# Performance work log

Measured on AMD Instinct MI355X. Metric: run time of the kernel, lower is better.

Reference implementation:

```python
import jax, jax.numpy as jnp
import numpy as np

B, T, D = 1, 4096, 2048
NUM_HEADS, NUM_KV_HEADS, HEAD_DIM = 16, 8, 128
QUERY_PRE_ATTN_SCALAR = HEAD_DIM ** -0.5
SOFT_CAP = 50.0
WINDOW = 1024
ROPE_BASE = 10000.0
ROPE_SCALE = 1.0
K_MASK = -2.3819763e+38


def apply_rope(x, positions, head_dim, max_wavelength=ROPE_BASE, scale_factor=ROPE_SCALE):
    # x: [B, T, N, H], positions: [B, T]
    fraction = 2.0 * jnp.arange(head_dim // 2, dtype=jnp.float32) / head_dim
    timescale = max_wavelength ** fraction  # [H/2]
    sinusoid = positions[..., None].astype(jnp.float32) / timescale  # [B, T, H/2]
    sinusoid = (sinusoid / scale_factor)[..., None, :]  # [B, T, 1, H/2]
    sin, cos = jnp.sin(sinusoid), jnp.cos(sinusoid)
    first, second = jnp.split(x, 2, axis=-1)
    out = jnp.concatenate([first * cos - second * sin,
                           second * cos + first * sin], axis=-1)
    return out.astype(x.dtype)


def setup_inputs() -> dict:
    key = jax.random.key(0)
    ks = jax.random.split(key, 4)
    x = jax.random.normal(ks[0], (B, T, D), dtype=jnp.float32)
    segment_pos = jnp.broadcast_to(jnp.arange(T, dtype=jnp.int32), (B, T))
    # causal mask [B, T, S]
    attn_mask = jnp.broadcast_to(
        jnp.tril(jnp.ones((T, T), dtype=jnp.bool_)), (B, T, T))
    q_w = jax.random.normal(ks[1], (NUM_HEADS, D, HEAD_DIM), dtype=jnp.float32) * 0.02
    kv_w = jax.random.normal(ks[2], (2, NUM_KV_HEADS, D, HEAD_DIM), dtype=jnp.float32) * 0.02
    o_w = jax.random.normal(ks[3], (NUM_HEADS, HEAD_DIM, D), dtype=jnp.float32) * 0.02
    return {"x": x, "segment_pos": segment_pos, "attn_mask": attn_mask,
            "q_w": q_w, "kv_w": kv_w, "o_w": o_w}


def reference(x, segment_pos, attn_mask, q_w, kv_w, o_w):
    # Projections (GQA: separate q and kv einsums)
    q = jnp.einsum('BTD,NDH->BTNH', x, q_w)          # [B,T,N,H]
    k = jnp.einsum('BSD,KDH->BSKH', x, kv_w[0])      # [B,S,K,H]
    v = jnp.einsum('BSD,KDH->BSKH', x, kv_w[1])      # [B,S,K,H]

    q = apply_rope(q, segment_pos, HEAD_DIM)
    q = q * QUERY_PRE_ATTN_SCALAR
    k = apply_rope(k, segment_pos, HEAD_DIM)

    num_groups = NUM_HEADS // NUM_KV_HEADS
    qg = q.reshape(B, T, NUM_KV_HEADS, num_groups, HEAD_DIM)
    logits = jnp.einsum('BTKGH,BSKH->BTKGS', qg, k)
    logits = logits.reshape(B, T, NUM_HEADS, -1)     # [B,T,N,S]

    # soft cap
    logits = jnp.tanh(logits / SOFT_CAP) * SOFT_CAP

    # sliding-window mask combined with causal mask
    all_ones = jnp.ones_like(attn_mask)
    sliding = jnp.triu(all_ones, -WINDOW + 1) * jnp.tril(all_ones, WINDOW - 1)
    mask = sliding * attn_mask                       # [B,T,S] bool

    padded = jnp.where(mask[:, :, None, :], logits, K_MASK)
    probs = jax.nn.softmax(padded, axis=-1).astype(k.dtype)

    probs_g = probs.reshape(B, T, NUM_KV_HEADS, num_groups, -1)
    encoded = jnp.einsum('BTKGS,BSKH->BTKGH', probs_g, v)
    encoded = encoded.reshape(B, T, NUM_HEADS, HEAD_DIM)

    attn_output = jnp.einsum('BTNH,NHD->BTD', encoded, o_w)
    return attn_output
```

## Files before the change

### kernel.cpp

```cpp
#include <hip/hip_runtime.h>
#include <hip/hip_bf16.h>
#include <math.h>

typedef __attribute__((ext_vector_type(8))) short short8;
typedef __attribute__((ext_vector_type(8))) unsigned short ushort8;
typedef __attribute__((ext_vector_type(4))) float f32x4;
typedef __attribute__((ext_vector_type(2))) float f32x2;

#define T_SEQ 4096
#define D_MODEL 2048
#define N_HEADS 16
#define N_KV 8
#define HEAD_DIM 128
#define QSCALE 0.08838834764831845f

__device__ __forceinline__ float bf2f(unsigned short u) {
  union { unsigned int i; float f; } x; x.i = ((unsigned int)u) << 16; return x.f;
}
__device__ __forceinline__ unsigned short f2bf(float f) {
  union { float f; unsigned int i; } x; x.f = f;
  unsigned int i = x.i;
  unsigned int r = i + 0x7fffu + ((i >> 16) & 1u);
  return (unsigned short)(r >> 16);
}

__global__ __launch_bounds__(256) void prep_kernel(const float* __restrict__ x,
                                                   unsigned short* __restrict__ xb,
                                                   const int* __restrict__ segpos,
                                                   float2* __restrict__ tab) {
  int b = blockIdx.x;
  if (b < 4096) {
    int idx = b * 256 + threadIdx.x;
    const float4* p = reinterpret_cast<const float4*>(x) + (size_t)idx * 2;
    float4 a = p[0], c = p[1];
    ushort8 o;
    o[0] = f2bf(a.x); o[1] = f2bf(a.y); o[2] = f2bf(a.z); o[3] = f2bf(a.w);
    o[4] = f2bf(c.x); o[5] = f2bf(c.y); o[6] = f2bf(c.z); o[7] = f2bf(c.w);
    reinterpret_cast<ushort8*>(xb)[idx] = o;
  } else {
    int idx = (b - 4096) * 256 + threadIdx.x;
    int t = idx >> 6, i = idx & 63;
    float pos = (float)segpos[t];
    float ts = powf(10000.f, (float)(2 * i) / 128.f);
    float ang = pos / ts;
    tab[idx] = make_float2(sinf(ang), cosf(ang));
  }
}

__global__ __launch_bounds__(256) void wqkv_transpose_kernel(const float* __restrict__ q_w,
                                                             const float* __restrict__ kv_w,
                                                             unsigned short* __restrict__ Wt) {
  __shared__ float tile[32][33];
  int z = blockIdx.z;
  const float* src = (z < 16) ? q_w + (size_t)z * 2048 * 128
                              : kv_w + (size_t)(z - 16) * 2048 * 128;
  unsigned short* dst = Wt + (size_t)z * 128 * 2048;
  int c0 = blockIdx.x * 32, r0 = blockIdx.y * 32;
  int tx = threadIdx.x & 31, ty = threadIdx.x >> 5;
#pragma unroll
  for (int i = 0; i < 4; ++i)
    tile[ty + i * 8][tx] = src[(size_t)(r0 + ty + i * 8) * 128 + c0 + tx];
  __syncthreads();
#pragma unroll
  for (int i = 0; i < 4; ++i)
    dst[(size_t)(c0 + ty + i * 8) * 2048 + r0 + tx] = f2bf(tile[tx][ty + i * 8]);
}

#define G2L(gp, lp)                                                           \
  __builtin_amdgcn_global_load_lds(                                           \
      (const __attribute__((address_space(1))) void*)(gp),                    \
      (__attribute__((address_space(3))) void*)(lp), 16, 0, 0)
#define GBAR() asm volatile("s_barrier" ::: "memory")
#define VMW(n) asm volatile("s_waitcnt vmcnt(" #n ")" ::: "memory")
#define LG0()  asm volatile("s_waitcnt lgkmcnt(0)" ::: "memory")

template <int OUT_BF16>
__global__ __launch_bounds__(512, 2) void gemm256_kernel(const unsigned short* __restrict__ A,
                                                         const unsigned short* __restrict__ Bt,
                                                         void* __restrict__ Cout,
                                                         int M, int N, int K) {
  extern __shared__ unsigned short smem[];
  unsigned short* ldsA = smem;
  unsigned short* ldsB = smem + 32768;
  const int tid = threadIdx.x;
  const int lane = tid & 63, wave = tid >> 6;
  const int wm = wave >> 2, wn = wave & 3;
  const int lr = lane & 15, lg = lane >> 4;
  const int swz = (lr & 7) << 3;
  const int c0s = (lg * 8) ^ swz;
  const int c1s = (32 + lg * 8) ^ swz;

  int id = blockIdx.y * gridDim.x + blockIdx.x;
  int nb = gridDim.x * gridDim.y;
  int sw = (id & 7) * (nb >> 3) + (id >> 3);
  const long brow = (long)(sw / gridDim.x) * 256;
  const long bcol = (long)(sw % gridDim.x) * 256;

  const unsigned short* Ag = A + brow * K;
  const unsigned short* Bg = Bt + bcol * K;

  const int r0 = tid >> 3;
  const int cs = ((tid & 7) * 8) ^ ((r0 & 7) << 3);

#define ST_A(tt, b, a)                                                        \
  { G2L(Ag + (size_t)((a) * 128 + r0) * K + (size_t)(tt) * 64 + cs,           \
        ldsA + (b) * 16384 + (a) * 8192 + tid * 8);                           \
    G2L(Ag + (size_t)((a) * 128 + r0 + 64) * K + (size_t)(tt) * 64 + cs,      \
        ldsA + (b) * 16384 + (a) * 8192 + 4096 + tid * 8); }
#define ST_B(tt, b, h)                                                        \
  { G2L(Bg + (size_t)((h) * 128 + r0) * K + (size_t)(tt) * 64 + cs,           \
        ldsB + (b) * 16384 + (h) * 8192 + tid * 8);                           \
    G2L(Bg + (size_t)((h) * 128 + r0 + 64) * K + (size_t)(tt) * 64 + cs,      \
        ldsB + (b) * 16384 + (h) * 8192 + 4096 + tid * 8); }

  f32x4 acc[8][4] = {};
  short8 bf[4][2];
  short8 af[4];

#define RD_B(b)                                                               \
  { const unsigned short* pb = ldsB + (b) * 16384 + wn * 4096;                \
    _Pragma("unroll")                                                         \
    for (int n = 0; n < 4; ++n) {                                             \
      bf[n][0] = *(const short8*)(pb + (n * 16 + lr) * 64 + c0s);             \
      bf[n][1] = *(const short8*)(pb + (n * 16 + lr) * 64 + c1s);             \
    } }
#define RD_A(b, mb)                                                           \
  { const unsigned short* pa = ldsA + (b) * 16384 + wm * 8192;                \
    af[0] = *(const short8*)(pa + ((mb) * 16 + lr) * 64 + c0s);               \
    af[1] = *(const short8*)(pa + ((mb) * 16 + lr) * 64 + c1s);               \
    af[2] = *(const short8*)(pa + ((mb) * 16 + 16 + lr) * 64 + c0s);          \
    af[3] = *(const short8*)(pa + ((mb) * 16 + 16 + lr) * 64 + c1s); }
#define MFMA2(mb)                                                             \
  { __builtin_amdgcn_s_setprio(1);                                            \
    _Pragma("unroll")                                                         \
    for (int n = 0; n < 4; ++n) {                                             \
      acc[mb][n]     = __builtin_amdgcn_mfma_f32_16x16x32_bf16(af[0], bf[n][0], acc[mb][n], 0, 0, 0);     \
      acc[mb][n]     = __builtin_amdgcn_mfma_f32_16x16x32_bf16(af[1], bf[n][1], acc[mb][n], 0, 0, 0);     \
      acc[mb + 1][n] = __builtin_amdgcn_mfma_f32_16x16x32_bf16(af[2], bf[n][0], acc[mb + 1][n], 0, 0, 0); \
      acc[mb + 1][n] = __builtin_amdgcn_mfma_f32_16x16x32_bf16(af[3], bf[n][1], acc[mb + 1][n], 0, 0, 0); \
    }                                                                         \
    __builtin_amdgcn_s_setprio(0); }

  const int NT = K >> 6;
  ST_B(0, 0, 0); ST_B(0, 0, 1); ST_A(0, 0, 0); ST_A(0, 0, 1);
  ST_B(1, 1, 0); ST_B(1, 1, 1);
  VMW(4); GBAR();
  for (int j = 0; j < (NT >> 1); ++j) {
    const int c1 = 2 * j + 1, t2 = 2 * j + 2, t3 = 2 * j + 3;
    const bool s2 = t2 < NT, s3 = t3 < NT;
    RD_B(0); RD_A(0, 0); ST_A(c1, 1, 0);
    GBAR(); LG0(); MFMA2(0); GBAR();
    RD_A(0, 2); ST_A(c1, 1, 1);
    if (s2) ST_B(t2, 0, 0);
    GBAR(); MFMA2(2); GBAR();
    RD_A(0, 4);
    if (s2) ST_B(t2, 0, 1);
    GBAR(); MFMA2(4); GBAR();
    RD_A(0, 6);
    if (s2) { VMW(4); } else { VMW(0); }
    GBAR(); LG0(); MFMA2(6); GBAR();
    RD_B(1); RD_A(1, 0);
    if (s2) ST_A(t2, 0, 0);
    GBAR(); LG0(); MFMA2(0); GBAR();
    RD_A(1, 2);
    if (s2) ST_A(t2, 0, 1);
    if (s3) ST_B(t3, 1, 0);
    GBAR(); MFMA2(2); GBAR();
    RD_A(1, 4);
    if (s3) ST_B(t3, 1, 1);
    GBAR(); MFMA2(4); GBAR();
    RD_A(1, 6);
    if (s3) { VMW(4); } else { VMW(0); }
    GBAR(); LG0(); MFMA2(6); GBAR();
  }

#pragma unroll
  for (int m = 0; m < 8; ++m) {
#pragma unroll
    for (int i = 0; i < 4; ++i) {
      long row = brow + wm * 128 + m * 16 + lg * 4 + i;
#pragma unroll
      for (int n = 0; n < 4; ++n) {
        long col = bcol + wn * 64 + n * 16 + lr;
        if (OUT_BF16)
          ((unsigned short*)Cout)[row * N + col] = f2bf(acc[m][n][i]);
        else
          ((float*)Cout)[row * N + col] = acc[m][n][i];
      }
    }
  }
#undef ST_A
#undef ST_B
#undef RD_A
#undef RD_B
#undef MFMA2
}

__global__ __launch_bounds__(512, 1) void gemm_op3_kernel(const unsigned short* __restrict__ A,
                                                          const unsigned short* __restrict__ Bt,
                                                          float* __restrict__ Cout,
                                                          int M, int N, int K) {
  extern __shared__ unsigned short smem[];
  unsigned short* ldsA = smem;
  unsigned short* ldsB = smem + 3 * 8192;
  const int tid = threadIdx.x;
  const int lane = tid & 63, wave = tid >> 6;
  const int wm = wave >> 2, wn = wave & 3;
  const int lr = lane & 15, lg = lane >> 4;
  const int swz = (lr & 7) << 3;
  const int c0s = (lg * 8) ^ swz;
  const int c1s = (32 + lg * 8) ^ swz;

  int id = blockIdx.y * gridDim.x + blockIdx.x;
  int sw = (id & 7) * 32 + (id >> 3);
  int c = sw >> 5, l = sw & 31;
  const long brow = (long)((c >> 2) * 16 + (l & 15)) * 128;
  const long bcol = (long)((c & 3) * 2 + (l >> 4)) * 256;

  const unsigned short* Ag = A + brow * K;
  const unsigned short* Bg = Bt + bcol * K;

  const int r0 = tid >> 3;
  const int cs = ((tid & 7) * 8) ^ ((r0 & 7) << 3);

#define ST_A3(tt, b)                                                          \
  { G2L(Ag + (size_t)(r0) * K + (size_t)(tt) * 64 + cs,                       \
        ldsA + (b) * 8192 + tid * 8);                                         \
    G2L(Ag + (size_t)(r0 + 64) * K + (size_t)(tt) * 64 + cs,                  \
        ldsA + (b) * 8192 + 4096 + tid * 8); }
#define ST_B3(tt, b, h)                                                       \
  { G2L(Bg + (size_t)((h) * 128 + r0) * K + (size_t)(tt) * 64 + cs,           \
        ldsB + (b) * 16384 + (h) * 8192 + tid * 8);                           \
    G2L(Bg + (size_t)((h) * 128 + r0 + 64) * K + (size_t)(tt) * 64 + cs,      \
        ldsB + (b) * 16384 + (h) * 8192 + 4096 + tid * 8); }

  f32x4 acc[4][4] = {};
  short8 bf[4][2];
  short8 af0[4], af1[4];

#define RD_B3(b)                                                              \
  { const unsigned short* pb = ldsB + (b) * 16384 + wn * 4096;                \
    _Pragma("unroll")                                                         \
    for (int n = 0; n < 4; ++n) {                                             \
      bf[n][0] = *(const short8*)(pb + (n * 16 + lr) * 64 + c0s);             \
      bf[n][1] = *(const short8*)(pb + (n * 16 + lr) * 64 + c1s);             \
    } }
#define RD_A3(b, mb, dst)                                                     \
  { const unsigned short* pa = ldsA + (b) * 8192 + wm * 4096;                 \
    dst[0] = *(const short8*)(pa + ((mb) * 16 + lr) * 64 + c0s);              \
    dst[1] = *(const short8*)(pa + ((mb) * 16 + lr) * 64 + c1s);              \
    dst[2] = *(const short8*)(pa + ((mb) * 16 + 16 + lr) * 64 + c0s);         \
    dst[3] = *(const short8*)(pa + ((mb) * 16 + 16 + lr) * 64 + c1s); }
#define MFMA2X(mb, afx)                                                       \
  { _Pragma("unroll")                                                         \
    for (int n = 0; n < 4; ++n) {                                             \
      acc[mb][n]     = __builtin_amdgcn_mfma_f32_16x16x32_bf16(afx[0], bf[n][0], acc[mb][n], 0, 0, 0);     \
      acc[mb][n]     = __builtin_amdgcn_mfma_f32_16x16x32_bf16(afx[1], bf[n][1], acc[mb][n], 0, 0, 0);     \
      acc[mb + 1][n] = __builtin_amdgcn_mfma_f32_16x16x32_bf16(afx[2], bf[n][0], acc[mb + 1][n], 0, 0, 0); \
      acc[mb + 1][n] = __builtin_amdgcn_mfma_f32_16x16x32_bf16(afx[3], bf[n][1], acc[mb + 1][n], 0, 0, 0); \
    } }

  const int NT = K >> 6;
  ST_B3(0, 0, 0); ST_B3(0, 0, 1); ST_A3(0, 0);
  ST_B3(1, 1, 0); ST_B3(1, 1, 1); ST_A3(1, 1);
  VMW(6); GBAR();
  int b = 0;
  for (int t = 0; t < NT; ++t) {
    int bn = b + 2; if (bn >= 3) bn -= 3;
    const bool st = (t + 2) < NT;
    RD_B3(b); RD_A3(b, 0, af0); RD_A3(b, 2, af1);
    if (st) { ST_B3(t + 2, bn, 0); ST_B3(t + 2, bn, 1); ST_A3(t + 2, bn); VMW(6); }
    else    { VMW(0); }
    GBAR(); LG0();
    __builtin_amdgcn_s_setprio(1);
    MFMA2X(0, af0); MFMA2X(2, af1);
    __builtin_amdgcn_s_setprio(0);
    GBAR();
    b = b + 1; if (b >= 3) b = 0;
  }

#pragma unroll
  for (int m = 0; m < 4; ++m) {
#pragma unroll
    for (int i = 0; i < 4; ++i) {
      long row = brow + wm * 64 + m * 16 + lg * 4 + i;
#pragma unroll
      for (int n = 0; n < 4; ++n) {
        long col = bcol + wn * 64 + n * 16 + lr;
        Cout[row * N + col] = acc[m][n][i];
      }
    }
  }
#undef ST_A3
#undef ST_B3
#undef RD_A3
#undef RD_B3
#undef MFMA2X
}

__global__ __launch_bounds__(256) void rope_vt_ow_kernel(const unsigned short* __restrict__ raw,
                                                         const float2* __restrict__ tab,
                                                         unsigned short* __restrict__ Qb,
                                                         unsigned short* __restrict__ Kb,
                                                         unsigned short* __restrict__ Vt,
                                                         const float* __restrict__ o_w,
                                                         unsigned short* __restrict__ o_wt) {
  __shared__ unsigned short tileU[32][33];
  __shared__ float tileF[32][33];
  int b = blockIdx.x;
  if (b < 3072) {
    int gid = b * 256 + threadIdx.x;
    int j = gid & 7;
    int rem = gid >> 3;
    int hs = rem % 24;
    int t = rem / 24;
    int i0 = j * 8;
    float sv[8], cv[8];
    const float2* tp = tab + t * 64 + i0;
#pragma unroll
    for (int q = 0; q < 8; ++q) { float2 sc2 = tp[q]; sv[q] = sc2.x; cv[q] = sc2.y; }
    if (hs < 16) {
      const unsigned short* p = raw + (size_t)t * 4096 + hs * 128 + i0;
      ushort8 a = *(const ushort8*)p;
      ushort8 c = *(const ushort8*)(p + 64);
      ushort8 o1, o2;
#pragma unroll
      for (int q = 0; q < 8; ++q) {
        float fa = bf2f(a[q]), fb = bf2f(c[q]);
        o1[q] = f2bf((fa * cv[q] - fb * sv[q]) * QSCALE);
        o2[q] = f2bf((fb * cv[q] + fa * sv[q]) * QSCALE);
      }
      unsigned short* qp = Qb + ((size_t)hs * T_SEQ + t) * 128 + i0;
      *(ushort8*)qp = o1;
      *(ushort8*)(qp + 64) = o2;
    } else {
      int kn = hs - 16;
      const unsigned short* p = raw + (size_t)t * 4096 + 2048 + kn * 128 + i0;
      ushort8 a = *(const ushort8*)p;
      ushort8 c = *(const ushort8*)(p + 64);
      ushort8 o1, o2;
#pragma unroll
      for (int q = 0; q < 8; ++q) {
        float fa = bf2f(a[q]), fb = bf2f(c[q]);
        o1[q] = f2bf(fa * cv[q] - fb * sv[q]);
        o2[q] = f2bf(fb * cv[q] + fa * sv[q]);
      }
      unsigned short* kp = Kb + ((size_t)kn * T_SEQ + t) * 128 + i0;
      *(ushort8*)kp = o1;
      *(ushort8*)(kp + 64) = o2;
    }
  } else if (b < 7168) {
    int id = b - 3072;
    int bx = id & 3, by = (id >> 2) & 127, bz = id >> 9;
    const unsigned short* src = raw + 3072 + (size_t)bz * 128;
    unsigned short* dst = Vt + (size_t)bz * 128 * 4096;
    int c0 = bx * 32, r0 = by * 32;
    int tx = threadIdx.x & 31, ty = threadIdx.x >> 5;
#pragma unroll
    for (int i = 0; i < 4; ++i)
      tileU[ty + i * 8][tx] = src[(size_t)(r0 + ty + i * 8) * 4096 + c0 + tx];
    __syncthreads();
#pragma unroll
    for (int i = 0; i < 4; ++i)
      dst[(size_t)(c0 + ty + i * 8) * 4096 + r0 + tx] = tileU[tx][ty + i * 8];
  } else {
    int id = b - 7168;
    int bx = id & 63, by = id >> 6;
    int c0 = bx * 32, r0 = by * 32;
    int tx = threadIdx.x & 31, ty = threadIdx.x >> 5;
#pragma unroll
    for (int i = 0; i < 4; ++i)
      tileF[ty + i * 8][tx] = o_w[(size_t)(r0 + ty + i * 8) * 2048 + c0 + tx];
    __syncthreads();
#pragma unroll
    for (int i = 0; i < 4; ++i)
      o_wt[(size_t)(c0 + ty + i * 8) * 2048 + r0 + tx] = f2bf(tileF[tx][ty + i * 8]);
  }
}

__global__ __launch_bounds__(512, 2) void attn_kernel(const unsigned short* __restrict__ Qb,
                                                      const unsigned short* __restrict__ Kb,
                                                      const unsigned short* __restrict__ Vt,
                                                      unsigned short* __restrict__ enc) {
  __shared__ unsigned short Ks[2][64][128];
  __shared__ unsigned short Vs[2][128][64];
  __shared__ unsigned short Ps[8][32][72];
  int rawb = blockIdx.x;
  int lin = (rawb & 7) * 32 + (rawb >> 3);
  const int h = lin >> 4;
  const int qb0 = (lin & 15) * 256;
  const int kvh = h >> 1;
  const int tid = threadIdx.x, lane = tid & 63, wave = tid >> 6;
  const int qw = qb0 + wave * 32;
  const int lr = lane & 15, lg = lane >> 4;
  const int sw = (lr & 7) << 3;
  const int ck0 = (lg * 8) ^ sw, ck1 = (32 + lg * 8) ^ sw;
  const int ck2 = (64 + lg * 8) ^ sw, ck3 = (96 + lg * 8) ^ sw;

  short8 aq[2][4];
#pragma unroll
  for (int g = 0; g < 2; ++g) {
    const unsigned short* qp = Qb + ((size_t)h * T_SEQ + qw + g * 16 + lr) * 128 + lg * 8;
#pragma unroll
    for (int c = 0; c < 4; ++c) aq[g][c] = *(const short8*)(qp + c * 32);
  }
  f32x4 acc[2][8] = {};
  float lsum[2] = {0.f, 0.f};

  const int s_lo = (qb0 - 1023) > 0 ? (qb0 - 1023) : 0;
  const int kb_lo = s_lo >> 6, kb_hi = (qb0 + 255) >> 6;

  const int rK = tid >> 4;
  const int cpK = (tid & 15) * 8;
  const int colK = cpK ^ ((rK & 7) << 3);
  const int rV = tid >> 3;
  const int cpV = (tid & 7) * 8;
  const int colV = cpV ^ ((rV & 7) << 3);
  const unsigned short* kgb = Kb + ((size_t)kvh * T_SEQ + rK) * 128 + colK;
  const unsigned short* vgb = Vt + ((size_t)kvh * 128 + rV) * T_SEQ + colV;

  ushort8 kr0, kr1, vr0, vr1;
  {
    const int s0g = kb_lo * 64;
    kr0 = *(const ushort8*)(kgb + (size_t)s0g * 128);
    kr1 = *(const ushort8*)(kgb + (size_t)(s0g + 32) * 128);
    vr0 = *(const ushort8*)(vgb + s0g);
    vr1 = *(const ushort8*)(vgb + (size_t)64 * T_SEQ + s0g);
  }

  const int qg0 = qw + lr, qg1 = qw + 16 + lr;
  for (int kb = kb_lo; kb <= kb_hi; ++kb) {
    const int s0g = kb * 64;
    const int buf = kb & 1;
    *(ushort8*)&Ks[buf][rK][cpK] = kr0;
    *(ushort8*)&Ks[buf][rK + 32][cpK] = kr1;
    *(ushort8*)&Vs[buf][rV][cpV] = vr0;
    *(ushort8*)&Vs[buf][rV + 64][cpV] = vr1;
    __syncthreads();
    if (kb < kb_hi) {
      const int sn = s0g + 64;
      kr0 = *(const ushort8*)(kgb + (size_t)sn * 128);
      kr1 = *(const ushort8*)(kgb + (size_t)(sn + 32) * 128);
      vr0 = *(const ushort8*)(vgb + sn);
      vr1 = *(const ushort8*)(vgb + (size_t)64 * T_SEQ + sn);
    }
    if (s0g > qw + 31 || s0g + 63 < qw - 1023) continue;
    const bool interior = (s0g + 63 <= qw) && (s0g >= qw - 992);

    f32x4 sT0[4] = {}, sT1[4] = {};
    __builtin_amdgcn_s_setprio(1);
#pragma unroll
    for (int st = 0; st < 4; ++st) {
      const unsigned short* kp = &Ks[buf][st * 16 + lr][0];
      short8 k0 = *(const short8*)(kp + ck0);
      short8 k1 = *(const short8*)(kp + ck1);
      short8 k2 = *(const short8*)(kp + ck2);
      short8 k3 = *(const short8*)(kp + ck3);
      sT0[st] = __builtin_amdgcn_mfma_f32_16x16x32_bf16(k0, aq[0][0], sT0[st], 0, 0, 0);
      sT1[st] = __builtin_amdgcn_mfma_f32_16x16x32_bf16(k0, aq[1][0], sT1[st], 0, 0, 0);
      sT0[st] = __builtin_amdgcn_mfma_f32_16x16x32_bf16(k1, aq[0][1], sT0[st], 0, 0, 0);
      sT1[st] = __builtin_amdgcn_mfma_f32_16x16x32_bf16(k1, aq[1][1], sT1[st], 0, 0, 0);
      sT0[st] = __builtin_amdgcn_mfma_f32_16x16x32_bf16(k2, aq[0][2], sT0[st], 0, 0, 0);
      sT1[st] = __builtin_amdgcn_mfma_f32_16x16x32_bf16(k2, aq[1][2], sT1[st], 0, 0, 0);
      sT0[st] = __builtin_amdgcn_mfma_f32_16x16x32_bf16(k3, aq[0][3], sT0[st], 0, 0, 0);
      sT1[st] = __builtin_amdgcn_mfma_f32_16x16x32_bf16(k3, aq[1][3], sT1[st], 0, 0, 0);
    }
    __builtin_amdgcn_s_setprio(0);

#pragma unroll
    for (int g = 0; g < 2; ++g) {
      const f32x4* sTg = g ? sT1 : sT0;
      const int qgg = g ? qg1 : qg0;
#pragma unroll
      for (int st = 0; st < 4; ++st) {
        f32x4 svv = sTg[st];
        f32x2 sa, sb;
        sa[0] = svv[0]; sa[1] = svv[1]; sb[0] = svv[2]; sb[1] = svv[3];
        f32x2 ua = sa * sa, ub = sb * sb;
        f32x2 numa = ua * 4.0e-4f + 15.f, numb = ub * 4.0e-4f + 15.f;
        f32x2 dena = ua * 2.4e-3f + 15.f, denb = ub * 2.4e-3f + 15.f;
        f32x2 ra, rb;
        ra[0] = __builtin_amdgcn_rcpf(dena[0]); ra[1] = __builtin_amdgcn_rcpf(dena[1]);
        rb[0] = __builtin_amdgcn_rcpf(denb[0]); rb[1] = __builtin_amdgcn_rcpf(denb[1]);
        f32x2 ea = (sa * 1.44269504f) * numa * ra;
        f32x2 eb = (sb * 1.44269504f) * numb * rb;
        float e[4] = {ea[0], ea[1], eb[0], eb[1]};
        float p[4];
#pragma unroll
        for (int r = 0; r < 4; ++r) {
          if (!interior) {
            int sg = s0g + st * 16 + lg * 4 + r;
            e[r] = ((unsigned)(qgg - sg) <= 1023u) ? e[r] : -__builtin_inff();
          }
          asm("v_exp_f32 %0, %1" : "=v"(p[r]) : "v"(e[r]));
        }
        lsum[g] += (p[0] + p[1]) + (p[2] + p[3]);
        unsigned u0, u1;
        asm("v_cvt_pk_bf16_f32 %0, %1, %2" : "=v"(u0) : "v"(p[0]), "v"(p[1]));
        asm("v_cvt_pk_bf16_f32 %0, %1, %2" : "=v"(u1) : "v"(p[2]), "v"(p[3]));
        uint2 w; w.x = u0; w.y = u1;
        *(uint2*)&Ps[wave][g * 16 + lr][st * 16 + lg * 4] = w;
      }
    }
    short8 pa00 = *(const short8*)&Ps[wave][lr][lg * 8];
    short8 pa01 = *(const short8*)&Ps[wave][lr][32 + lg * 8];
    short8 pa10 = *(const short8*)&Ps[wave][16 + lr][lg * 8];
    short8 pa11 = *(const short8*)&Ps[wave][16 + lr][32 + lg * 8];
    __builtin_amdgcn_s_setprio(1);
#pragma unroll
    for (int d0 = 0; d0 < 8; ++d0) {
      const unsigned short* vp = &Vs[buf][d0 * 16 + lr][0];
      short8 bv0 = *(const short8*)(vp + ((lg * 8) ^ sw));
      short8 bv1 = *(const short8*)(vp + ((32 + lg * 8) ^ sw));
      acc[0][d0] = __builtin_amdgcn_mfma_f32_16x16x32_bf16(pa00, bv0, acc[0][d0], 0, 0, 0);
      acc[1][d0] = __builtin_amdgcn_mfma_f32_16x16x32_bf16(pa10, bv0, acc[1][d0], 0, 0, 0);
      acc[0][d0] = __builtin_amdgcn_mfma_f32_16x16x32_bf16(pa01, bv1, acc[0][d0], 0, 0, 0);
      acc[1][d0] = __builtin_amdgcn_mfma_f32_16x16x32_bf16(pa11, bv1, acc[1][d0], 0, 0, 0);
    }
    __builtin_amdgcn_s_setprio(0);
  }

#pragma unroll
  for (int g = 0; g < 2; ++g) {
    float l = lsum[g];
    l += __shfl_xor(l, 16);
    l += __shfl_xor(l, 32);
#pragma unroll
    for (int r = 0; r < 4; ++r) {
      float lt = __shfl(l, lg * 4 + r);
      float inv = __builtin_amdgcn_rcpf(lt);
      int row = qw + g * 16 + lg * 4 + r;
      unsigned short* op = enc + (size_t)row * D_MODEL + h * 128 + lr;
#pragma unroll
      for (int d0 = 0; d0 < 8; ++d0) op[d0 * 16] = f2bf(acc[g][d0][r] * inv);
    }
  }
}

extern "C" void kernel_launch(void* const* d_in, const int* in_sizes, int n_in,
                              void* d_out, int out_size, void* d_ws, size_t ws_size,
                              hipStream_t stream) {
  const float* x = (const float*)d_in[0];
  const int* segpos = (const int*)d_in[1];
  const float* q_w = (const float*)d_in[3];
  const float* kv_w = (const float*)d_in[4];
  const float* o_w = (const float*)d_in[5];
  float* out = (float*)d_out;
  char* ws = (char*)d_ws;

  const size_t OFF_XB = 0;
  const size_t OFF_WT = OFF_XB + 16777216;
  const size_t OFF_RAW = OFF_WT + 16777216;
  const size_t OFF_KB = OFF_RAW + 33554432;
  const size_t OFF_VT = OFF_KB + 8388608;
  const size_t OFF_TAB = OFF_VT + 8388608;
  unsigned short* xb = (unsigned short*)(ws + OFF_XB);
  unsigned short* Wt = (unsigned short*)(ws + OFF_WT);
  unsigned short* raw = (unsigned short*)(ws + OFF_RAW);
  unsigned short* Kb = (unsigned short*)(ws + OFF_KB);
  unsigned short* Vt = (unsigned short*)(ws + OFF_VT);
  float2* tab = (float2*)(ws + OFF_TAB);
  unsigned short* o_wt = xb;
  unsigned short* Qb = Wt;
  unsigned short* enc = raw;

  hipFuncSetAttribute((const void*)(gemm256_kernel<1>),
                      hipFuncAttributeMaxDynamicSharedMemorySize, 131072);
  hipFuncSetAttribute((const void*)gemm_op3_kernel,
                      hipFuncAttributeMaxDynamicSharedMemorySize, 147456);

  prep_kernel<<<dim3(5120), dim3(256), 0, stream>>>(x, xb, segpos, tab);
  wqkv_transpose_kernel<<<dim3(4, 64, 32), dim3(256), 0, stream>>>(q_w, kv_w, Wt);
  gemm256_kernel<1><<<dim3(16, 16), dim3(512), 131072, stream>>>(xb, Wt, (void*)raw, 4096, 4096, 2048);
  rope_vt_ow_kernel<<<dim3(11264), dim3(256), 0, stream>>>(raw, tab, Qb, Kb, Vt, o_w, o_wt);
  attn_kernel<<<dim3(256), dim3(512), 0, stream>>>(Qb, Kb, Vt, enc);
  gemm_op3_kernel<<<dim3(8, 32), dim3(512), 147456, stream>>>(enc, o_wt, out, 4096, 2048, 2048);
}
```

Baseline: 198.4 us.

## Shrink output-projection GEMM tiles to 128x128 with double buffering and fuse prep kernels

Replaces the 128x256 triple-buffered output-projection GEMM with a 128x128 tile, double-buffered variant using 64KB LDS and launch bounds allowing more resident blocks. The grid doubles to 512 blocks, which should fill the device's compute units better, at the cost of lower per-block operand reuse and less prefetch depth. It also merges the weight transpose into the input bf16/rope-table prep kernel, removing one kernel launch.

```diff
diff --git a/kernel.cpp b/kernel.cpp
--- a/kernel.cpp
+++ b/kernel.cpp
@@ -24,10 +24,14 @@
   return (unsigned short)(r >> 16);
 }
 
-__global__ __launch_bounds__(256) void prep_kernel(const float* __restrict__ x,
-                                                   unsigned short* __restrict__ xb,
-                                                   const int* __restrict__ segpos,
-                                                   float2* __restrict__ tab) {
+__global__ __launch_bounds__(256) void prep2_kernel(const float* __restrict__ x,
+                                                    unsigned short* __restrict__ xb,
+                                                    const int* __restrict__ segpos,
+                                                    float2* __restrict__ tab,
+                                                    const float* __restrict__ q_w,
+                                                    const float* __restrict__ kv_w,
+                                                    unsigned short* __restrict__ Wt) {
+  __shared__ float tile[32][33];
   int b = blockIdx.x;
   if (b < 4096) {
     int idx = b * 256 + threadIdx.x;
@@ -37,33 +41,30 @@
     o[0] = f2bf(a.x); o[1] = f2bf(a.y); o[2] = f2bf(a.z); o[3] = f2bf(a.w);
     o[4] = f2bf(c.x); o[5] = f2bf(c.y); o[6] = f2bf(c.z); o[7] = f2bf(c.w);
     reinterpret_cast<ushort8*>(xb)[idx] = o;
-  } else {
+  } else if (b < 5120) {
     int idx = (b - 4096) * 256 + threadIdx.x;
     int t = idx >> 6, i = idx & 63;
     float pos = (float)segpos[t];
     float ts = powf(10000.f, (float)(2 * i) / 128.f);
     float ang = pos / ts;
     tab[idx] = make_float2(sinf(ang), cosf(ang));
-  }
-}
-
-__global__ __launch_bounds__(256) void wqkv_transpose_kernel(const float* __restrict__ q_w,
-                                                             const float* __restrict__ kv_w,
-                                                             unsigned short* __restrict__ Wt) {
-  __shared__ float tile[32][33];
-  int z = blockIdx.z;
-  const float* src = (z < 16) ? q_w + (size_t)z * 2048 * 128
-                              : kv_w + (size_t)(z - 16) * 2048 * 128;
-  unsigned short* dst = Wt + (size_t)z * 128 * 2048;
-  int c0 = blockIdx.x * 32, r0 = blockIdx.y * 32;
-  int tx = threadIdx.x & 31, ty = threadIdx.x >> 5;
-#pragma unroll
-  for (int i = 0; i < 4; ++i)
-    tile[ty + i * 8][tx] = src[(size_t)(r0 + ty + i * 8) * 128 + c0 + tx];
-  __syncthreads();
-#pragma unroll
-  for (int i = 0; i < 4; ++i)
-    dst[(size_t)(c0 + ty + i * 8) * 2048 + r0 + tx] = f2bf(tile[tx][ty + i * 8]);
+  } else {
+    int id = b - 5120;
+    int z = id >> 8, rem = id & 255;
+    int bx = rem & 3, by = rem >> 2;
+    const float* src = (z < 16) ? q_w + (size_t)z * 2048 * 128
+                                : kv_w + (size_t)(z - 16) * 2048 * 128;
+    unsigned short* dst = Wt + (size_t)z * 128 * 2048;
+    int c0 = bx * 32, r0 = by * 32;
+    int tx = threadIdx.x & 31, ty = threadIdx.x >> 5;
+#pragma unroll
+    for (int i = 0; i < 4; ++i)
+      tile[ty + i * 8][tx] = src[(size_t)(r0 + ty + i * 8) * 128 + c0 + tx];
+    __syncthreads();
+#pragma unroll
+    for (int i = 0; i < 4; ++i)
+      dst[(size_t)(c0 + ty + i * 8) * 2048 + r0 + tx] = f2bf(tile[tx][ty + i * 8]);
+  }
 }
 
 #define G2L(gp, lp)                                                           \
@@ -196,13 +197,13 @@
 #undef MFMA2
 }
 
-__global__ __launch_bounds__(512, 1) void gemm_op3_kernel(const unsigned short* __restrict__ A,
-                                                          const unsigned short* __restrict__ Bt,
-                                                          float* __restrict__ Cout,
-                                                          int M, int N, int K) {
+__global__ __launch_bounds__(512, 4) void gemm_o2_kernel(const unsigned short* __restrict__ A,
+                                                         const unsigned short* __restrict__ Bt,
+                                                         float* __restrict__ Cout,
+                                                         int M, int N, int K) {
   extern __shared__ unsigned short smem[];
   unsigned short* ldsA = smem;
-  unsigned short* ldsB = smem + 3 * 8192;
+  unsigned short* ldsB = smem + 16384;
   const int tid = threadIdx.x;
   const int lane = tid & 63, wave = tid >> 6;
   const int wm = wave >> 2, wn = wave & 3;
@@ -212,10 +213,9 @@
   const int c1s = (32 + lg * 8) ^ swz;
 
   int id = blockIdx.y * gridDim.x + blockIdx.x;
-  int sw = (id & 7) * 32 + (id >> 3);
-  int c = sw >> 5, l = sw & 31;
-  const long brow = (long)((c >> 2) * 16 + (l & 15)) * 128;
-  const long bcol = (long)((c & 3) * 2 + (l >> 4)) * 256;
+  int sw = (id & 7) * 64 + (id >> 3);
+  const long brow = (long)(sw / 16) * 128;
+  const long bcol = (long)(sw % 16) * 128;
 
   const unsigned short* Ag = A + brow * K;
   const unsigned short* Bg = Bt + bcol * K;
@@ -223,61 +223,53 @@
   const int r0 = tid >> 3;
   const int cs = ((tid & 7) * 8) ^ ((r0 & 7) << 3);
 
-#define ST_A3(tt, b)                                                          \
+#define ST2(tt, b)                                                            \
   { G2L(Ag + (size_t)(r0) * K + (size_t)(tt) * 64 + cs,                       \
         ldsA + (b) * 8192 + tid * 8);                                         \
     G2L(Ag + (size_t)(r0 + 64) * K + (size_t)(tt) * 64 + cs,                  \
-        ldsA + (b) * 8192 + 4096 + tid * 8); }
-#define ST_B3(tt, b, h)                                                       \
-  { G2L(Bg + (size_t)((h) * 128 + r0) * K + (size_t)(tt) * 64 + cs,           \
-        ldsB + (b) * 16384 + (h) * 8192 + tid * 8);                           \
-    G2L(Bg + (size_t)((h) * 128 + r0 + 64) * K + (size_t)(tt) * 64 + cs,      \
-        ldsB + (b) * 16384 + (h) * 8192 + 4096 + tid * 8); }
-
-  f32x4 acc[4][4] = {};
-  short8 bf[4][2];
-  short8 af0[4], af1[4];
-
-#define RD_B3(b)                                                              \
-  { const unsigned short* pb = ldsB + (b) * 16384 + wn * 4096;                \
-    _Pragma("unroll")                                                         \
-    for (int n = 0; n < 4; ++n) {                                             \
-      bf[n][0] = *(const short8*)(pb + (n * 16 + lr) * 64 + c0s);             \
-      bf[n][1] = *(const short8*)(pb + (n * 16 + lr) * 64 + c1s);             \
-    } }
-#define RD_A3(b, mb, dst)                                                     \
-  { const unsigned short* pa = ldsA + (b) * 8192 + wm * 4096;                 \
-    dst[0] = *(const short8*)(pa + ((mb) * 16 + lr) * 64 + c0s);              \
-    dst[1] = *(const short8*)(pa + ((mb) * 16 + lr) * 64 + c1s);              \
-    dst[2] = *(const short8*)(pa + ((mb) * 16 + 16 + lr) * 64 + c0s);         \
-    dst[3] = *(const short8*)(pa + ((mb) * 16 + 16 + lr) * 64 + c1s); }
-#define MFMA2X(mb, afx)                                                       \
-  { _Pragma("unroll")                                                         \
-    for (int n = 0; n < 4; ++n) {                                             \
-      acc[mb][n]     = __builtin_amdgcn_mfma_f32_16x16x32_bf16(afx[0], bf[n][0], acc[mb][n], 0, 0, 0);     \
-      acc[mb][n]     = __builtin_amdgcn_mfma_f32_16x16x32_bf16(afx[1], bf[n][1], acc[mb][n], 0, 0, 0);     \
-      acc[mb + 1][n] = __builtin_amdgcn_mfma_f32_16x16x32_bf16(afx[2], bf[n][0], acc[mb + 1][n], 0, 0, 0); \
-      acc[mb + 1][n] = __builtin_amdgcn_mfma_f32_16x16x32_bf16(afx[3], bf[n][1], acc[mb + 1][n], 0, 0, 0); \
-    } }
+        ldsA + (b) * 8192 + 4096 + tid * 8);                                  \
+    G2L(Bg + (size_t)(r0) * K + (size_t)(tt) * 64 + cs,                       \
+        ldsB + (b) * 8192 + tid * 8);                                         \
+    G2L(Bg + (size_t)(r0 + 64) * K + (size_t)(tt) * 64 + cs,                  \
+        ldsB + (b) * 8192 + 4096 + tid * 8); }
+
+  f32x4 acc[4][2] = {};
+  short8 af[2][4];
+  short8 bf[2][2];
 
   const int NT = K >> 6;
-  ST_B3(0, 0, 0); ST_B3(0, 0, 1); ST_A3(0, 0);
-  ST_B3(1, 1, 0); ST_B3(1, 1, 1); ST_A3(1, 1);
-  VMW(6); GBAR();
-  int b = 0;
+  ST2(0, 0);
   for (int t = 0; t < NT; ++t) {
-    int bn = b + 2; if (bn >= 3) bn -= 3;
-    const bool st = (t + 2) < NT;
-    RD_B3(b); RD_A3(b, 0, af0); RD_A3(b, 2, af1);
-    if (st) { ST_B3(t + 2, bn, 0); ST_B3(t + 2, bn, 1); ST_A3(t + 2, bn); VMW(6); }
-    else    { VMW(0); }
-    GBAR(); LG0();
+    const int buf = t & 1;
+    if (t + 1 < NT) { ST2(t + 1, buf ^ 1); VMW(4); } else { VMW(0); }
+    GBAR();
+    {
+      const unsigned short* pa = ldsA + buf * 8192 + wm * 4096;
+      const unsigned short* pb = ldsB + buf * 8192 + wn * 2048;
+#pragma unroll
+      for (int m = 0; m < 4; ++m) {
+        af[0][m] = *(const short8*)(pa + (m * 16 + lr) * 64 + c0s);
+        af[1][m] = *(const short8*)(pa + (m * 16 + lr) * 64 + c1s);
+      }
+#pragma unroll
+      for (int n = 0; n < 2; ++n) {
+        bf[0][n] = *(const short8*)(pb + (n * 16 + lr) * 64 + c0s);
+        bf[1][n] = *(const short8*)(pb + (n * 16 + lr) * 64 + c1s);
+      }
+    }
+    LG0();
     __builtin_amdgcn_s_setprio(1);
-    MFMA2X(0, af0); MFMA2X(2, af1);
+#pragma unroll
+    for (int kc = 0; kc < 2; ++kc)
+#pragma unroll
+      for (int m = 0; m < 4; ++m)
+#pragma unroll
+        for (int n = 0; n < 2; ++n)
+          acc[m][n] = __builtin_amdgcn_mfma_f32_16x16x32_bf16(af[kc][m], bf[kc][n], acc[m][n], 0, 0, 0);
     __builtin_amdgcn_s_setprio(0);
     GBAR();
-    b = b + 1; if (b >= 3) b = 0;
-  }
+  }
+#undef ST2
 
 #pragma unroll
   for (int m = 0; m < 4; ++m) {
@@ -285,17 +277,12 @@
     for (int i = 0; i < 4; ++i) {
       long row = brow + wm * 64 + m * 16 + lg * 4 + i;
 #pragma unroll
-      for (int n = 0; n < 4; ++n) {
-        long col = bcol + wn * 64 + n * 16 + lr;
+      for (int n = 0; n < 2; ++n) {
+        long col = bcol + wn * 32 + n * 16 + lr;
         Cout[row * N + col] = acc[m][n][i];
       }
     }
   }
-#undef ST_A3
-#undef ST_B3
-#undef RD_A3
-#undef RD_B3
-#undef MFMA2X
 }
 
 __global__ __launch_bounds__(256) void rope_vt_ow_kernel(const unsigned short* __restrict__ raw,
@@ -566,13 +553,12 @@
 
   hipFuncSetAttribute((const void*)(gemm256_kernel<1>),
                       hipFuncAttributeMaxDynamicSharedMemorySize, 131072);
-  hipFuncSetAttribute((const void*)gemm_op3_kernel,
-                      hipFuncAttributeMaxDynamicSharedMemorySize, 147456);
-
-  prep_kernel<<<dim3(5120), dim3(256), 0, stream>>>(x, xb, segpos, tab);
-  wqkv_transpose_kernel<<<dim3(4, 64, 32), dim3(256), 0, stream>>>(q_w, kv_w, Wt);
+  hipFuncSetAttribute((const void*)gemm_o2_kernel,
+                      hipFuncAttributeMaxDynamicSharedMemorySize, 65536);
+
+  prep2_kernel<<<dim3(13312), dim3(256), 0, stream>>>(x, xb, segpos, tab, q_w, kv_w, Wt);
   gemm256_kernel<1><<<dim3(16, 16), dim3(512), 131072, stream>>>(xb, Wt, (void*)raw, 4096, 4096, 2048);
   rope_vt_ow_kernel<<<dim3(11264), dim3(256), 0, stream>>>(raw, tab, Qb, Kb, Vt, o_w, o_wt);
   attn_kernel<<<dim3(256), dim3(512), 0, stream>>>(Qb, Kb, Vt, enc);
-  gemm_op3_kernel<<<dim3(8, 32), dim3(512), 147456, stream>>>(enc, o_wt, out, 4096, 2048, 2048);
-}
+  gemm_o2_kernel<<<dim3(16, 32), dim3(512), 65536, stream>>>(enc, o_wt, out, 4096, 2048, 2048);
+}
```

Result: no change. 199.0 us (+0.3%).
